# Kernel tuning notes

Hardware: AMD Instinct MI355X
Metric: run time of the kernel (lower is better)

Reference implementation:

```python
import jax, jax.numpy as jnp
import numpy as np

B, S, D = 4, 2048, 1024
E, K = 8, 2
H = 4 * D  # expert hidden (expansion=4)


def setup_inputs() -> dict:
    key = jax.random.key(0)
    ks = jax.random.split(key, 5)
    x = jax.random.normal(ks[0], (B, S, D), dtype=jnp.float32)
    Wr = jax.random.normal(ks[1], (E, D), dtype=jnp.float32) * 0.02
    br = jnp.zeros((E,), dtype=jnp.float32)
    W1 = jax.random.normal(ks[2], (E, H, D), dtype=jnp.float32) * 0.02
    b1 = jnp.zeros((E, H), dtype=jnp.float32)
    W2 = jax.random.normal(ks[3], (E, D, H), dtype=jnp.float32) * 0.02
    b2 = jnp.zeros((E, D), dtype=jnp.float32)
    return {"x": x, "Wr": Wr, "br": br, "W1": W1, "b1": b1, "W2": W2, "b2": b2}


def reference(x, Wr, br, W1, b1, W2, b2):
    # Dropout is inactive (eval mode). torch Linear: y = x @ W.T + b.
    Bb, Ss, Dm = x.shape
    xf = x.reshape(-1, Dm)                       # [T, D], T = B*S
    logits = xf @ Wr.T + br                      # [T, E]
    probs = jax.nn.softmax(logits, axis=-1)      # [T, E]
    topw, topi = jax.lax.top_k(probs, K)         # [T, K]
    topw = topw / jnp.sum(topw, axis=-1, keepdims=True)
    # combine weights per (token, expert): sum over k slots of renormalized weight
    comb = jnp.sum(jax.nn.one_hot(topi, E, dtype=xf.dtype) * topw[..., None], axis=1)  # [T, E]
    # dense per-expert MLP over all tokens, then weighted combine
    h = jax.nn.gelu(jnp.einsum('td,ehd->eth', xf, W1) + b1[:, None, :], approximate=False)  # [E, T, 4D]
    oe = jnp.einsum('eth,edh->etd', h, W2) + b2[:, None, :]                                  # [E, T, D]
    out = jnp.einsum('te,etd->td', comb, oe)     # [T, D]
    return out.reshape(Bb, Ss, Dm)
```

## Files before the change

### kernel.cpp

```cpp
#include <hip/hip_runtime.h>

#define T_TOK 8192
#define DMODEL 1024
#define NEXP 8
#define TOPK 2
#define HID 4096
#define NPAIR (T_TOK*TOPK)
#define BM 128
#define BN 128
#define BK 64
#define MAXT (NPAIR/128 + NEXP)

typedef unsigned short u16;
typedef unsigned int u32;
typedef short s16x8 __attribute__((ext_vector_type(8)));
typedef float f32x4 __attribute__((ext_vector_type(4)));

__device__ __forceinline__ u16 f2b(float f) {
    union { float f; unsigned int u; } v; v.f = f;
    return (u16)((v.u + 0x7fffu + ((v.u >> 16) & 1u)) >> 16);
}
__device__ __forceinline__ float b2f(u16 h) {
    union { unsigned int u; float f; } v; v.u = ((unsigned int)h) << 16;
    return v.f;
}

__device__ __forceinline__ s16x8 cvt8(float4 f0, float4 f1) {
    s16x8 o;
    o[0]=(short)f2b(f0.x); o[1]=(short)f2b(f0.y); o[2]=(short)f2b(f0.z); o[3]=(short)f2b(f0.w);
    o[4]=(short)f2b(f1.x); o[5]=(short)f2b(f1.y); o[6]=(short)f2b(f1.z); o[7]=(short)f2b(f1.w);
    return o;
}

__device__ __forceinline__ void gload16(const void* g, void* l) {
    __builtin_amdgcn_global_load_lds(
        (const __attribute__((address_space(1))) unsigned int*)g,
        (__attribute__((address_space(3))) unsigned int*)l, 16, 0, 0);
}

__device__ __forceinline__ float gelu_fast(float v) {
    float y = 0.7978845608028654f * v * fmaf(0.044715f * v, v, 1.0f);
    float t = -2.8853900817779268f * y;
    float z, r;
    asm("v_exp_f32 %0, %1" : "=v"(z) : "v"(t));
    float den = 1.0f + z;
    asm("v_rcp_f32 %0, %1" : "=v"(r) : "v"(den));
    return v * r;
}

__device__ __forceinline__ int xcd_swz(int bid, int nact) {
    int q = nact >> 3, r = nact & 7;
    int xcd = bid & 7, i = bid >> 3;
    return (xcd < r ? xcd * (q + 1) : r * (q + 1) + (xcd - r) * q) + i;
}

__global__ __launch_bounds__(256) void router_kernel(
    const float* __restrict__ x, const float* __restrict__ Wr, const float* __restrict__ br,
    int* __restrict__ topi, float* __restrict__ topw,
    u16* __restrict__ xb, const float* __restrict__ W1, u16* __restrict__ W1b)
{
    __shared__ float WrS[NEXP * DMODEL];
    int tid = threadIdx.x;
    const float4* Wr4 = (const float4*)Wr;
    float4* WrS4 = (float4*)WrS;
    for (int i = tid; i < NEXP * DMODEL / 4; i += 256) WrS4[i] = Wr4[i];
    __syncthreads();

    int wid = tid >> 6, lane = tid & 63;
    int t = blockIdx.x * 4 + wid;
    const float* xr = x + (size_t)t * DMODEL;

    float acc[NEXP];
#pragma unroll
    for (int e = 0; e < NEXP; ++e) acc[e] = 0.f;
#pragma unroll 4
    for (int i = lane; i < DMODEL; i += 64) {
        float xv = xr[i];
#pragma unroll
        for (int e = 0; e < NEXP; ++e) acc[e] = fmaf(xv, WrS[e * DMODEL + i], acc[e]);
    }
#pragma unroll
    for (int e = 0; e < NEXP; ++e) {
        float v = acc[e];
#pragma unroll
        for (int off = 32; off > 0; off >>= 1) v += __shfl_xor(v, off);
        acc[e] = v;
    }
    if (lane == 0) {
        float lg[NEXP];
#pragma unroll
        for (int e = 0; e < NEXP; ++e) lg[e] = acc[e] + br[e];
        int i1 = 0;
#pragma unroll
        for (int e = 1; e < NEXP; ++e) if (lg[e] > lg[i1]) i1 = e;
        int i2 = (i1 == 0) ? 1 : 0;
#pragma unroll
        for (int e = 0; e < NEXP; ++e) if (e != i1 && lg[e] > lg[i2]) i2 = e;
        float e2 = expf(lg[i2] - lg[i1]);
        float s = 1.f + e2;
        topi[t * 2] = i1;  topi[t * 2 + 1] = i2;
        topw[t * 2] = 1.f / s;  topw[t * 2 + 1] = e2 / s;
    }

    {
        const float* xblk = x + (size_t)blockIdx.x * 4 * DMODEL;
        u16* xbblk = xb + (size_t)blockIdx.x * 4 * DMODEL;
#pragma unroll
        for (int i = tid; i < 4 * DMODEL / 8; i += 256) {
            const float4* p = (const float4*)(xblk + i * 8);
            *(s16x8*)(xbblk + i * 8) = cvt8(p[0], p[1]);
        }
    }

    long n8 = (long)NEXP * DMODEL * HID / 8;
    long stride = (long)gridDim.x * 256;
    for (long i = (long)blockIdx.x * 256 + tid; i < n8; i += stride) {
        const float4* p = (const float4*)(W1 + i * 8);
        float4 f0 = p[0], f1 = p[1];
        *(s16x8*)(W1b + i * 8) = cvt8(f0, f1);
    }
}

__global__ __launch_bounds__(256) void count_offsets_kernel(
    const int* __restrict__ topi, int* __restrict__ cnt, int* __restrict__ offs,
    u32* __restrict__ table, int* __restrict__ meta)
{
    __shared__ int red[NEXP * 256];
    int tid = threadIdx.x;
    int c[NEXP] = {};
    for (int i = tid; i < NPAIR; i += 256) {
        int e = topi[i];
#pragma unroll
        for (int k = 0; k < NEXP; ++k) c[k] += (e == k) ? 1 : 0;
    }
#pragma unroll
    for (int k = 0; k < NEXP; ++k) red[k * 256 + tid] = c[k];
    __syncthreads();
    if (tid < NEXP) {
        int s = 0;
        for (int i = 0; i < 256; ++i) s += red[tid * 256 + i];
        cnt[tid] = s;
    }
    __syncthreads();
    if (tid == 0) {
        int a = 0;
        for (int e = 0; e < NEXP; ++e) { offs[e] = a; a += cnt[e]; }
        offs[NEXP] = a;
        int nt = 0;
        for (int e = 0; e < NEXP; ++e)
            for (int r0 = 0; r0 < cnt[e]; r0 += 128)
                table[nt++] = ((u32)e << 20) | (u32)r0;
        meta[0] = nt;
    }
}

__global__ __launch_bounds__(256) void scatter_kernel(
    const int* __restrict__ topi, const float* __restrict__ topw,
    const int* __restrict__ offs, int* __restrict__ fill,
    int* __restrict__ tok, float* __restrict__ wgt, int* __restrict__ pos)
{
    int t = blockIdx.x * 256 + threadIdx.x;
    int lane = threadIdx.x & 63;
#pragma unroll
    for (int s = 0; s < TOPK; ++s) {
        int e = topi[t * 2 + s];
        float w = topw[t * 2 + s];
#pragma unroll
        for (int ex = 0; ex < NEXP; ++ex) {
            unsigned long long m = __ballot(e == ex);
            if (e == ex) {
                int ldr = (int)__ffsll((unsigned long long)m) - 1;
                int base = 0;
                if (lane == ldr) base = atomicAdd(&fill[ex * 32], (int)__popcll(m));
                base = __shfl(base, ldr);
                int mypos = base + (int)__popcll(m & ((1ull << lane) - 1ull));
                int p = offs[ex] + mypos;
                tok[p] = t;
                wgt[p] = w;
                pos[t * 2 + s] = p;
            }
        }
    }
}

__global__ __launch_bounds__(256) void combine_kernel(
    const u16* __restrict__ Op, const int* __restrict__ pos, float* __restrict__ out)
{
    int tid = threadIdx.x;
    int t = blockIdx.x * 2 + (tid >> 7);
    int c = (tid & 127) * 8;
    int pa = pos[t * 2], pb = pos[t * 2 + 1];
    s16x8 a = *(const s16x8*)(Op + (size_t)pa * DMODEL + c);
    s16x8 b = *(const s16x8*)(Op + (size_t)pb * DMODEL + c);
    float* o = out + (size_t)t * DMODEL + c;
    float4 o0, o1;
    o0.x = b2f((u16)a[0]) + b2f((u16)b[0]);
    o0.y = b2f((u16)a[1]) + b2f((u16)b[1]);
    o0.z = b2f((u16)a[2]) + b2f((u16)b[2]);
    o0.w = b2f((u16)a[3]) + b2f((u16)b[3]);
    o1.x = b2f((u16)a[4]) + b2f((u16)b[4]);
    o1.y = b2f((u16)a[5]) + b2f((u16)b[5]);
    o1.z = b2f((u16)a[6]) + b2f((u16)b[6]);
    o1.w = b2f((u16)a[7]) + b2f((u16)b[7]);
    ((float4*)o)[0] = o0;
    ((float4*)o)[1] = o1;
}

#define STAGE_TILE(koff) do {                                               \
    _Pragma("unroll") for (int c = 0; c < 4; ++c) {                         \
        int idx = c * 256 + tid;                                            \
        gload16(Agp + aoffA[c] + (size_t)(koff), (char*)As + idx * 16);     \
        gload16(Bgp + boffB[c] + (size_t)(koff), (char*)Bs + idx * 16);     \
    }                                                                       \
} while (0)

#define COMPUTE_TILE() do {                                                 \
    _Pragma("unroll") for (int half = 0; half < 2; ++half) {                \
        s16x8 av[4], bv[4];                                                 \
        int kslot = half * 4 + (lane >> 4);                                 \
        _Pragma("unroll") for (int mi = 0; mi < 4; ++mi) {                  \
            int rr = wm * 64 + mi * 16 + (lane & 15);                       \
            av[mi] = *(const s16x8*)((char*)As + rr * 128 + ((kslot ^ (rr & 7)) * 16)); } \
        _Pragma("unroll") for (int nf = 0; nf < 4; ++nf) {                  \
            int rb = wn * 64 + nf * 16 + (lane & 15);                       \
            bv[nf] = *(const s16x8*)((char*)Bs + rb * 128 + ((kslot ^ (rb & 7)) * 16)); } \
        _Pragma("unroll") for (int mi = 0; mi < 4; ++mi)                    \
        _Pragma("unroll") for (int nf = 0; nf < 4; ++nf)                    \
            acc[mi][nf] = __builtin_amdgcn_mfma_f32_16x16x32_bf16(          \
                av[mi], bv[nf], acc[mi][nf], 0, 0, 0);                      \
    }                                                                       \
} while (0)

#define VM0() asm volatile("s_waitcnt vmcnt(0)" ::: "memory")

#define M97_LOOP(NT, KBASE) do {                                            \
    _Pragma("unroll 1")                                                     \
    for (int t = 0; t < (NT); ++t) {                                        \
        STAGE_TILE((size_t)(KBASE) + (size_t)t * BK);                       \
        VM0();                                                              \
        __syncthreads();                                                    \
        COMPUTE_TILE();                                                     \
        __syncthreads();                                                    \
    }                                                                       \
} while (0)

#define CHUNK_RS(c)                                                         \
    int r##c = ((c) * 256 + tid) >> 3;                                      \
    int s##c = (tid & 7) ^ (r##c & 7);

__global__ __launch_bounds__(256, 3) void gemm1_kernel(
    const u16* __restrict__ xb, const u16* __restrict__ W1b, const float* __restrict__ b1,
    const int* __restrict__ tok, const int* __restrict__ cnt, const int* __restrict__ offs,
    const u32* __restrict__ table, const int* __restrict__ meta,
    u16* __restrict__ H1, int p0, int p1,
    const float* __restrict__ W2, u16* __restrict__ W2b)
{
    __shared__ __align__(16) u16 As[BM * BK];
    __shared__ __align__(16) u16 Bs[BN * BK];
    const int tid = threadIdx.x;
    const int lane = tid & 63, wid = tid >> 6;
    const int wm = wid >> 1, wn = wid & 1;

    const int NCOL = HID / BN;
    int nt = meta[0];
    int nact = NCOL * nt;
    int bid = blockIdx.x;
    bool active = (bid < nact);
    int e = 0, row0 = 0, ce = 0, oe = 0, col0 = 0;
    if (active) {
        int swz = xcd_swz(bid, nact);
        int tile = swz / NCOL, colb = swz & (NCOL - 1);
        u32 entry = table[tile];
        e = (int)(entry >> 20);
        row0 = (int)(entry & 0xFFFFFu);
        ce = cnt[e]; oe = offs[e];
        col0 = colb * BN;
        active = !(oe + min(ce, row0 + BM) <= p0 || oe + row0 >= p1);
    }

    if (active) {
        f32x4 acc[4][4] = {};
        const u16* Agp = xb;
        const u16* Bgp = W1b;
        size_t aoffA[4], boffB[4];
        {
            CHUNK_RS(0) CHUNK_RS(1) CHUNK_RS(2) CHUNK_RS(3)
#define TOKA(rc) ((row0 + (rc)) < ce ? tok[oe + row0 + (rc)] : tok[oe])
            aoffA[0] = (size_t)TOKA(r0) * DMODEL + s0 * 8;
            aoffA[1] = (size_t)TOKA(r1) * DMODEL + s1 * 8;
            aoffA[2] = (size_t)TOKA(r2) * DMODEL + s2 * 8;
            aoffA[3] = (size_t)TOKA(r3) * DMODEL + s3 * 8;
#undef TOKA
            boffB[0] = ((size_t)e * HID + col0 + r0) * DMODEL + s0 * 8;
            boffB[1] = ((size_t)e * HID + col0 + r1) * DMODEL + s1 * 8;
            boffB[2] = ((size_t)e * HID + col0 + r2) * DMODEL + s2 * 8;
            boffB[3] = ((size_t)e * HID + col0 + r3) * DMODEL + s3 * 8;
        }

        M97_LOOP(DMODEL / BK, 0);

        float bias[4];
#pragma unroll
        for (int nf = 0; nf < 4; ++nf)
            bias[nf] = b1[e * HID + col0 + wn * 64 + nf * 16 + (lane & 15)];

#pragma unroll
        for (int mf = 0; mf < 4; ++mf) {
#pragma unroll
            for (int j = 0; j < 4; ++j) {
                int r = wm * 64 + mf * 16 + ((lane >> 4) * 4) + j;
                int gi = row0 + r;
                int p = oe + gi;
                if (gi < ce && p >= p0 && p < p1) {
                    u16* hrow = H1 + (size_t)(p - p0) * HID;
#pragma unroll
                    for (int nf = 0; nf < 4; ++nf) {
                        int n = col0 + wn * 64 + nf * 16 + (lane & 15);
                        hrow[n] = f2b(gelu_fast(acc[mf][nf][j] + bias[nf]));
                    }
                }
            }
        }
    }

    if (p0 == 0) {
        long n8 = (long)NEXP * DMODEL * HID / 8;
        long stride = (long)gridDim.x * 256;
        for (long i = (long)bid * 256 + tid; i < n8; i += stride) {
            const float4* p = (const float4*)(W2 + i * 8);
            float4 f0 = p[0], f1 = p[1];
            *(s16x8*)(W2b + i * 8) = cvt8(f0, f1);
        }
    }
}

__global__ __launch_bounds__(256, 3) void gemm2_kernel(
    const u16* __restrict__ H1, const u16* __restrict__ W2b, const float* __restrict__ b2,
    const float* __restrict__ wgt,
    const int* __restrict__ cnt, const int* __restrict__ offs,
    const u32* __restrict__ table, const int* __restrict__ meta,
    u16* __restrict__ Opair, int p0, int p1)
{
    __shared__ __align__(16) u16 As[BM * BK];
    __shared__ __align__(16) u16 Bs[BN * BK];
    const int tid = threadIdx.x;
    const int lane = tid & 63, wid = tid >> 6;
    const int wm = wid >> 1, wn = wid & 1;

    const int NCOL = DMODEL / BN;
    int nt = meta[0];
    int nact = NCOL * nt;
    int bid = blockIdx.x;
    if (bid >= nact) return;
    int swz = xcd_swz(bid, nact);
    int tile = swz >> 3, colb = swz & 7;
    u32 entry = table[tile];
    const int e = (int)(entry >> 20);
    const int row0 = (int)(entry & 0xFFFFFu);
    const int ce = cnt[e], oe = offs[e];
    if (oe + min(ce, row0 + BM) <= p0 || oe + row0 >= p1) return;
    const int col0 = colb * BN;

    f32x4 acc[4][4] = {};

    const u16* Agp = H1;
    const u16* Bgp = W2b;
    const int smax = p1 - p0 - 1;
    size_t aoffA[4], boffB[4];
    {
        CHUNK_RS(0) CHUNK_RS(1) CHUNK_RS(2) CHUNK_RS(3)
#define AIDX(rc) ({ int ai_ = oe + row0 + (rc) - p0;                         \
                    ai_ < 0 ? 0 : (ai_ > smax ? smax : ai_); })
        aoffA[0] = (size_t)AIDX(r0) * HID + s0 * 8;
        aoffA[1] = (size_t)AIDX(r1) * HID + s1 * 8;
        aoffA[2] = (size_t)AIDX(r2) * HID + s2 * 8;
        aoffA[3] = (size_t)AIDX(r3) * HID + s3 * 8;
#undef AIDX
        boffB[0] = ((size_t)e * DMODEL + col0 + r0) * HID + s0 * 8;
        boffB[1] = ((size_t)e * DMODEL + col0 + r1) * HID + s1 * 8;
        boffB[2] = ((size_t)e * DMODEL + col0 + r2) * HID + s2 * 8;
        boffB[3] = ((size_t)e * DMODEL + col0 + r3) * HID + s3 * 8;
    }

    M97_LOOP(HID / BK, 0);

    float bias[4];
#pragma unroll
    for (int nf = 0; nf < 4; ++nf)
        bias[nf] = b2[e * DMODEL + col0 + wn * 64 + nf * 16 + (lane & 15)];

#pragma unroll
    for (int mf = 0; mf < 4; ++mf) {
#pragma unroll
        for (int j = 0; j < 4; ++j) {
            int r = wm * 64 + mf * 16 + ((lane >> 4) * 4) + j;
            int gi = row0 + r;
            int p = oe + gi;
            if (gi < ce && p >= p0 && p < p1) {
                float w = wgt[p];
                u16* orow = Opair + (size_t)p * DMODEL;
#pragma unroll
                for (int nf = 0; nf < 4; ++nf) {
                    int n = col0 + wn * 64 + nf * 16 + (lane & 15);
                    orow[n] = f2b(w * (acc[mf][nf][j] + bias[nf]));
                }
            }
        }
    }
}

extern "C" void kernel_launch(void* const* d_in, const int* in_sizes, int n_in,
                              void* d_out, int out_size, void* d_ws, size_t ws_size,
                              hipStream_t stream)
{
    const float* x  = (const float*)d_in[0];
    const float* Wr = (const float*)d_in[1];
    const float* br = (const float*)d_in[2];
    const float* W1 = (const float*)d_in[3];
    const float* b1 = (const float*)d_in[4];
    const float* W2 = (const float*)d_in[5];
    const float* b2 = (const float*)d_in[6];
    float* out = (float*)d_out;

    char* ws = (char*)d_ws;
    u16* xb = (u16*)ws;
    size_t o2 = (size_t)T_TOK * DMODEL * 2;
    int*   cnt   = (int*)(ws + o2);
    int*   offs  = (int*)(ws + o2 + 64);
    int*   meta  = (int*)(ws + o2 + 192);
    u32*   table = (u32*)(ws + o2 + 256);
    int*   fill  = (int*)(ws + o2 + 1024);
    int*   topi  = (int*)(ws + o2 + 4096);
    float* topw  = (float*)(ws + o2 + 4096 + (size_t)NPAIR * 4);
    int*   tok   = (int*)(ws + o2 + 4096 + (size_t)NPAIR * 8);
    float* wgt   = (float*)(ws + o2 + 4096 + (size_t)NPAIR * 12);
    int*   pos   = (int*)(ws + o2 + 4096 + (size_t)NPAIR * 16);

    const size_t WBYTES = (size_t)NEXP * DMODEL * HID * 2;
    size_t oW2 = o2 + (2u << 20);
    size_t oW1 = oW2 + WBYTES;
    size_t oOp = oW1 + WBYTES;
    size_t oH  = oOp + (size_t)NPAIR * DMODEL * 2;
    u16* W2b   = (u16*)(ws + oW2);
    u16* W1b   = (u16*)(ws + oW1);
    u16* Opair = (u16*)(ws + oOp);
    u16* H1    = (u16*)(ws + oH);

    long long cap = ((long long)ws_size - (long long)oH) / ((long long)HID * 2);
    int slice = cap >= NPAIR ? NPAIR : (cap < 1024 ? 1024 : (int)cap);

    hipMemsetAsync(ws + o2, 0, 2048, stream);

    router_kernel<<<dim3(T_TOK / 4), 256, 0, stream>>>(x, Wr, br, topi, topw, xb, W1, W1b);
    count_offsets_kernel<<<dim3(1), 256, 0, stream>>>(topi, cnt, offs, table, meta);
    scatter_kernel<<<dim3(T_TOK / 256), 256, 0, stream>>>(topi, topw, offs, fill, tok, wgt, pos);

    for (int pp = 0; pp < NPAIR; pp += slice) {
        int p1v = pp + slice < NPAIR ? pp + slice : NPAIR;
        gemm1_kernel<<<dim3((HID / BN) * MAXT), 256, 0, stream>>>(
            xb, W1b, b1, tok, cnt, offs, table, meta, H1, pp, p1v, W2, W2b);
        gemm2_kernel<<<dim3((DMODEL / BN) * MAXT), 256, 0, stream>>>(
            H1, W2b, b2, wgt, cnt, offs, table, meta, Opair, pp, p1v);
    }

    combine_kernel<<<dim3(T_TOK / 2), 256, 0, stream>>>(Opair, pos, out);
}
```

Baseline: 495.1 us.

## Fuse W1 fp32-to-bf16 conversion into gemm1 tile loading

Removes the separate pass in the router kernel that converted all of W1 to bf16 in workspace. gemm1 now loads fp32 W1 directly into registers, converts it, and writes bf16 to shared memory, so the W1 write and re-read of a 64 MB bf16 copy go away. The cost is that each gemm1 tile reads twice as many bytes for B, and the re-reads across token tiles are now fp32. The B path also moves from async global-to-LDS loads to register staging.

```diff
diff --git a/kernel.cpp b/kernel.cpp
--- a/kernel.cpp
+++ b/kernel.cpp
@@ -56,8 +56,7 @@
 
 __global__ __launch_bounds__(256) void router_kernel(
     const float* __restrict__ x, const float* __restrict__ Wr, const float* __restrict__ br,
-    int* __restrict__ topi, float* __restrict__ topw,
-    u16* __restrict__ xb, const float* __restrict__ W1, u16* __restrict__ W1b)
+    int* __restrict__ topi, float* __restrict__ topw, u16* __restrict__ xb)
 {
     __shared__ float WrS[NEXP * DMODEL];
     int tid = threadIdx.x;
@@ -102,22 +101,12 @@
         topw[t * 2] = 1.f / s;  topw[t * 2 + 1] = e2 / s;
     }
 
-    {
-        const float* xblk = x + (size_t)blockIdx.x * 4 * DMODEL;
-        u16* xbblk = xb + (size_t)blockIdx.x * 4 * DMODEL;
-#pragma unroll
-        for (int i = tid; i < 4 * DMODEL / 8; i += 256) {
-            const float4* p = (const float4*)(xblk + i * 8);
-            *(s16x8*)(xbblk + i * 8) = cvt8(p[0], p[1]);
-        }
-    }
-
-    long n8 = (long)NEXP * DMODEL * HID / 8;
-    long stride = (long)gridDim.x * 256;
-    for (long i = (long)blockIdx.x * 256 + tid; i < n8; i += stride) {
-        const float4* p = (const float4*)(W1 + i * 8);
-        float4 f0 = p[0], f1 = p[1];
-        *(s16x8*)(W1b + i * 8) = cvt8(f0, f1);
+    const float* xblk = x + (size_t)blockIdx.x * 4 * DMODEL;
+    u16* xbblk = xb + (size_t)blockIdx.x * 4 * DMODEL;
+#pragma unroll
+    for (int i = tid; i < 4 * DMODEL / 8; i += 256) {
+        const float4* p = (const float4*)(xblk + i * 8);
+        *(s16x8*)(xbblk + i * 8) = cvt8(p[0], p[1]);
     }
 }
 
@@ -206,14 +195,6 @@
     ((float4*)o)[1] = o1;
 }
 
-#define STAGE_TILE(koff) do {                                               \
-    _Pragma("unroll") for (int c = 0; c < 4; ++c) {                         \
-        int idx = c * 256 + tid;                                            \
-        gload16(Agp + aoffA[c] + (size_t)(koff), (char*)As + idx * 16);     \
-        gload16(Bgp + boffB[c] + (size_t)(koff), (char*)Bs + idx * 16);     \
-    }                                                                       \
-} while (0)
-
 #define COMPUTE_TILE() do {                                                 \
     _Pragma("unroll") for (int half = 0; half < 2; ++half) {                \
         s16x8 av[4], bv[4];                                                 \
@@ -233,23 +214,12 @@
 
 #define VM0() asm volatile("s_waitcnt vmcnt(0)" ::: "memory")
 
-#define M97_LOOP(NT, KBASE) do {                                            \
-    _Pragma("unroll 1")                                                     \
-    for (int t = 0; t < (NT); ++t) {                                        \
-        STAGE_TILE((size_t)(KBASE) + (size_t)t * BK);                       \
-        VM0();                                                              \
-        __syncthreads();                                                    \
-        COMPUTE_TILE();                                                     \
-        __syncthreads();                                                    \
-    }                                                                       \
-} while (0)
-
 #define CHUNK_RS(c)                                                         \
     int r##c = ((c) * 256 + tid) >> 3;                                      \
     int s##c = (tid & 7) ^ (r##c & 7);
 
 __global__ __launch_bounds__(256, 3) void gemm1_kernel(
-    const u16* __restrict__ xb, const u16* __restrict__ W1b, const float* __restrict__ b1,
+    const u16* __restrict__ xb, const float* __restrict__ W1f, const float* __restrict__ b1,
     const int* __restrict__ tok, const int* __restrict__ cnt, const int* __restrict__ offs,
     const u32* __restrict__ table, const int* __restrict__ meta,
     u16* __restrict__ H1, int p0, int p1,
@@ -281,8 +251,9 @@
     if (active) {
         f32x4 acc[4][4] = {};
         const u16* Agp = xb;
-        const u16* Bgp = W1b;
-        size_t aoffA[4], boffB[4];
+        size_t aoffA[4];
+        size_t boffF[4];
+        int bws[4];
         {
             CHUNK_RS(0) CHUNK_RS(1) CHUNK_RS(2) CHUNK_RS(3)
 #define TOKA(rc) ((row0 + (rc)) < ce ? tok[oe + row0 + (rc)] : tok[oe])
@@ -291,13 +262,44 @@
             aoffA[2] = (size_t)TOKA(r2) * DMODEL + s2 * 8;
             aoffA[3] = (size_t)TOKA(r3) * DMODEL + s3 * 8;
 #undef TOKA
-            boffB[0] = ((size_t)e * HID + col0 + r0) * DMODEL + s0 * 8;
-            boffB[1] = ((size_t)e * HID + col0 + r1) * DMODEL + s1 * 8;
-            boffB[2] = ((size_t)e * HID + col0 + r2) * DMODEL + s2 * 8;
-            boffB[3] = ((size_t)e * HID + col0 + r3) * DMODEL + s3 * 8;
-        }
-
-        M97_LOOP(DMODEL / BK, 0);
+            boffF[0] = ((size_t)e * HID + col0 + r0) * DMODEL + s0 * 8;
+            boffF[1] = ((size_t)e * HID + col0 + r1) * DMODEL + s1 * 8;
+            boffF[2] = ((size_t)e * HID + col0 + r2) * DMODEL + s2 * 8;
+            boffF[3] = ((size_t)e * HID + col0 + r3) * DMODEL + s3 * 8;
+            bws[0] = r0 * 128 + (tid & 7) * 16;
+            bws[1] = r1 * 128 + (tid & 7) * 16;
+            bws[2] = r2 * 128 + (tid & 7) * 16;
+            bws[3] = r3 * 128 + (tid & 7) * 16;
+        }
+
+#pragma unroll 1
+        for (int t = 0; t < DMODEL / BK; ++t) {
+            const size_t k = (size_t)t * BK;
+            float4 bf0[2], bf1[2], bf2[2], bf3[2];
+            {
+                const float4* p0 = (const float4*)(W1f + boffF[0] + k);
+                const float4* p1 = (const float4*)(W1f + boffF[1] + k);
+                const float4* p2 = (const float4*)(W1f + boffF[2] + k);
+                const float4* p3 = (const float4*)(W1f + boffF[3] + k);
+                bf0[0] = p0[0]; bf0[1] = p0[1];
+                bf1[0] = p1[0]; bf1[1] = p1[1];
+                bf2[0] = p2[0]; bf2[1] = p2[1];
+                bf3[0] = p3[0]; bf3[1] = p3[1];
+            }
+#pragma unroll
+            for (int c = 0; c < 4; ++c) {
+                int idx = c * 256 + tid;
+                gload16(Agp + aoffA[c] + k, (char*)As + idx * 16);
+            }
+            VM0();
+            *(s16x8*)((char*)Bs + bws[0]) = cvt8(bf0[0], bf0[1]);
+            *(s16x8*)((char*)Bs + bws[1]) = cvt8(bf1[0], bf1[1]);
+            *(s16x8*)((char*)Bs + bws[2]) = cvt8(bf2[0], bf2[1]);
+            *(s16x8*)((char*)Bs + bws[3]) = cvt8(bf3[0], bf3[1]);
+            __syncthreads();
+            COMPUTE_TILE();
+            __syncthreads();
+        }
 
         float bias[4];
 #pragma unroll
@@ -382,7 +384,20 @@
         boffB[3] = ((size_t)e * DMODEL + col0 + r3) * HID + s3 * 8;
     }
 
-    M97_LOOP(HID / BK, 0);
+#pragma unroll 1
+    for (int t = 0; t < HID / BK; ++t) {
+        const size_t k = (size_t)t * BK;
+#pragma unroll
+        for (int c = 0; c < 4; ++c) {
+            int idx = c * 256 + tid;
+            gload16(Agp + aoffA[c] + k, (char*)As + idx * 16);
+            gload16(Bgp + boffB[c] + k, (char*)Bs + idx * 16);
+        }
+        VM0();
+        __syncthreads();
+        COMPUTE_TILE();
+        __syncthreads();
+    }
 
     float bias[4];
 #pragma unroll
@@ -438,11 +453,9 @@
 
     const size_t WBYTES = (size_t)NEXP * DMODEL * HID * 2;
     size_t oW2 = o2 + (2u << 20);
-    size_t oW1 = oW2 + WBYTES;
-    size_t oOp = oW1 + WBYTES;
+    size_t oOp = oW2 + WBYTES;
     size_t oH  = oOp + (size_t)NPAIR * DMODEL * 2;
     u16* W2b   = (u16*)(ws + oW2);
-    u16* W1b   = (u16*)(ws + oW1);
     u16* Opair = (u16*)(ws + oOp);
     u16* H1    = (u16*)(ws + oH);
 
@@ -451,14 +464,14 @@
 
     hipMemsetAsync(ws + o2, 0, 2048, stream);
 
-    router_kernel<<<dim3(T_TOK / 4), 256, 0, stream>>>(x, Wr, br, topi, topw, xb, W1, W1b);
+    router_kernel<<<dim3(T_TOK / 4), 256, 0, stream>>>(x, Wr, br, topi, topw, xb);
     count_offsets_kernel<<<dim3(1), 256, 0, stream>>>(topi, cnt, offs, table, meta);
     scatter_kernel<<<dim3(T_TOK / 256), 256, 0, stream>>>(topi, topw, offs, fill, tok, wgt, pos);
 
     for (int pp = 0; pp < NPAIR; pp += slice) {
         int p1v = pp + slice < NPAIR ? pp + slice : NPAIR;
         gemm1_kernel<<<dim3((HID / BN) * MAXT), 256, 0, stream>>>(
-            xb, W1b, b1, tok, cnt, offs, table, meta, H1, pp, p1v, W2, W2b);
+            xb, W1, b1, tok, cnt, offs, table, meta, H1, pp, p1v, W2, W2b);
         gemm2_kernel<<<dim3((DMODEL / BN) * MAXT), 256, 0, stream>>>(
             H1, W2b, b2, wgt, cnt, offs, table, meta, Opair, pp, p1v);
     }
```

Result: slower. 601.4 us (+21.5%).
